# Optimization experiments

Hardware: AMD Instinct MI355X
Metric: run time of the kernel (lower is better)

## Reference

```python
import jax, jax.numpy as jnp
import numpy as np

B, T, F, H = 256, 32, 128, 128
NUM_FILTERS, KH, KW, NUM_CLASSES = 64, 2, 2, 2
FLAT = NUM_FILTERS * (T - KH + 1) * (2 * F - KW + 1)  # 64*31*255 = 505920


def setup_inputs() -> dict:
    key = jax.random.key(0)
    ks = jax.random.split(key, 12)
    inp = {
        "X_nume": jax.random.normal(ks[0], (B, T, F), jnp.float32),
        "att_W": jax.random.uniform(ks[1], (F, H), jnp.float32),
        "att_U": jax.random.uniform(ks[2], (F, H), jnp.float32),
        "att_V": jax.random.uniform(ks[3], (H, 1), jnp.float32),
        "conv_w": jax.random.normal(ks[4], (NUM_FILTERS, 1, KH, KW), jnp.float32) * 0.5,
        "conv_b": jax.random.normal(ks[5], (NUM_FILTERS,), jnp.float32) * 0.1,
        "w1": jax.random.normal(ks[6], (FLAT, 256), jnp.float32) * (1.0 / np.sqrt(FLAT)),
        "b1": jnp.zeros((256,), jnp.float32),
        "w2": jax.random.normal(ks[7], (256, 32), jnp.float32) * (1.0 / np.sqrt(256)),
        "b2": jnp.zeros((32,), jnp.float32),
        "w3": jax.random.normal(ks[8], (32, NUM_CLASSES), jnp.float32) * (1.0 / np.sqrt(32)),
        "b3": jnp.zeros((NUM_CLASSES,), jnp.float32),
    }
    return inp


def reference(X_nume, att_W, att_U, att_V, conv_w, conv_b, w1, b1, w2, b2, w3, b3):
    X = X_nume  # [B, T, F]
    # --- additive attention, fully batched (replaces O(T^2) python loops) ---
    xw = jnp.einsum("btf,fh->bth", X, att_W)  # query proj [B,T,H]
    xu = jnp.einsum("btf,fh->bth", X, att_U)  # key proj   [B,T,H]
    # e[b,i,j] = V^T tanh(x_i W + x_j U)
    scores = jnp.squeeze(jnp.tanh(xw[:, :, None, :] + xu[:, None, :, :]) @ att_V, -1)  # [B,T,T]
    alpha = jax.nn.softmax(scores, axis=-1)  # softmax over j (includes diagonal)
    # context excludes j == i (original skips j == index AFTER softmax)
    mask = 1.0 - jnp.eye(T, dtype=X.dtype)
    c = jnp.einsum("bij,bjf->bif", alpha * mask, X)  # [B,T,F]
    feat = jnp.concatenate([X, c], axis=-1)  # [B,T,2F]
    # --- conv ---
    conv_in = feat[:, None, :, :]  # [B,1,T,2F]
    conv = jax.lax.conv_general_dilated(
        conv_in, conv_w, window_strides=(1, 1), padding="VALID",
        dimension_numbers=("NCHW", "OIHW", "NCHW"))
    conv = jax.nn.relu(conv + conv_b[None, :, None, None])  # [B,64,T-1,2F-1]
    # --- MLP head ---
    flat = conv.reshape(conv.shape[0], -1)
    h = jax.nn.relu(flat @ w1 + b1)
    h = jax.nn.relu(h @ w2 + b2)
    return h @ w3 + b3
```

## Files before the change

kernel.cpp:

```cpp
#include <hip/hip_runtime.h>
#include <hip/hip_bf16.h>

#define B_ 256
#define T_ 32
#define F_ 128
#define H_ 128
#define NF 64
#define OH 31
#define OW 255
#define POS_TOTAL (OH*OW)
#define N1 256
#define KT 248
#define NSTEPS 64

typedef __attribute__((ext_vector_type(8))) short bf16x8;
typedef __attribute__((ext_vector_type(4))) float f32x4;

__device__ __forceinline__ unsigned short f2bf_rne(float f) {
    unsigned int u = __float_as_uint(f);
    u += 0x7FFFu + ((u >> 16) & 1u);
    return (unsigned short)(u >> 16);
}

__global__ __launch_bounds__(256) void k_attn(
    const float* __restrict__ X, const float* __restrict__ W,
    const float* __restrict__ U, const float* __restrict__ V,
    float* __restrict__ featL)
{
    __shared__ float Xs[T_][F_];
    __shared__ float xw[T_][H_];
    __shared__ float xu[T_][H_];
    __shared__ float sc[T_][T_];
    __shared__ float Vs[H_];

    const int b = blockIdx.x;
    const int t = threadIdx.x;
    const float* Xb = X + (size_t)b * T_ * F_;

    for (int idx = t; idx < T_*F_; idx += 256) ((float*)Xs)[idx] = Xb[idx];
    if (t < H_) Vs[t] = V[t];
    __syncthreads();

    {
        const int h = t & 127, half = t >> 7;
        float aw[16], au[16];
        #pragma unroll
        for (int r = 0; r < 16; r++) { aw[r] = 0.f; au[r] = 0.f; }
        for (int f = 0; f < F_; f++) {
            const float wv = W[f*H_ + h];
            const float uv = U[f*H_ + h];
            #pragma unroll
            for (int r = 0; r < 16; r++) {
                const float xv = Xs[half*16 + r][f];
                aw[r] += xv * wv;
                au[r] += xv * uv;
            }
        }
        #pragma unroll
        for (int r = 0; r < 16; r++) {
            xw[half*16 + r][h] = aw[r];
            xu[half*16 + r][h] = au[r];
        }
    }
    __syncthreads();

    {
        const int i = t >> 3;
        const int j0 = (t & 7) * 4;
        float s0 = 0.f, s1 = 0.f, s2 = 0.f, s3 = 0.f;
        for (int h = 0; h < H_; h++) {
            const float xwv = xw[i][h];
            const float vv  = Vs[h];
            s0 += tanhf(xwv + xu[j0+0][h]) * vv;
            s1 += tanhf(xwv + xu[j0+1][h]) * vv;
            s2 += tanhf(xwv + xu[j0+2][h]) * vv;
            s3 += tanhf(xwv + xu[j0+3][h]) * vv;
        }
        sc[i][j0+0] = s0; sc[i][j0+1] = s1; sc[i][j0+2] = s2; sc[i][j0+3] = s3;
    }
    __syncthreads();

    if (t < T_) {
        float m = -1e30f;
        #pragma unroll
        for (int j = 0; j < T_; j++) m = fmaxf(m, sc[t][j]);
        float sum = 0.f;
        #pragma unroll
        for (int j = 0; j < T_; j++) sum += expf(sc[t][j] - m);
        const float inv = 1.f / sum;
        #pragma unroll
        for (int j = 0; j < T_; j++) {
            const float a = expf(sc[t][j] - m) * inv;
            sc[t][j] = (j == t) ? 0.f : a;
        }
    }
    __syncthreads();

    for (int idx = t; idx < T_*F_; idx += 256) {
        const int row = idx >> 7, f = idx & 127;
        float acc = 0.f;
        #pragma unroll
        for (int j = 0; j < T_; j++) acc += sc[row][j] * Xs[j][f];
        float* fr = featL + (size_t)b*8192 + row*256;
        fr[f]       = Xs[row][f];
        fr[128 + f] = acc;
    }
}

__global__ __launch_bounds__(256) void k_tr(
    const float* __restrict__ src, float* __restrict__ dst)
{
    __shared__ float tile[32][33];
    const int rc0 = blockIdx.x * 32;
    const int b0  = blockIdx.y * 32;
    const int tx = threadIdx.x & 31;
    const int ty = threadIdx.x >> 5;
    #pragma unroll
    for (int r = 0; r < 32; r += 8)
        tile[ty + r][tx] = src[(size_t)(b0 + ty + r)*8192 + rc0 + tx];
    __syncthreads();
    #pragma unroll
    for (int r = 0; r < 32; r += 8)
        dst[(size_t)(rc0 + ty + r)*256 + b0 + tx] = tile[tx][ty + r];
}

__global__ __launch_bounds__(512, 2) void k_gemm1(
    const float* __restrict__ featT, const float* __restrict__ cw,
    const float* __restrict__ cb, const float* __restrict__ w1,
    float* __restrict__ partial)
{
    __shared__ unsigned short As[2*4*256*8];
    __shared__ unsigned short Ws[2*4*256*8];
    __shared__ float cwL[256];
    __shared__ float cbL[64];

    const int t  = threadIdx.x;
    const int kt = blockIdx.x;

    if (t < 256) cwL[t] = cw[t];
    if (t < 64)  cbL[t] = cb[t];

    const int rn  = t & 255;
    const int fq2 = t >> 8;

    const int lane = t & 63, wid = t >> 6;
    const int wm = (wid >> 2) * 128;
    const int wn = (wid & 3) * 64;
    const int fr = lane & 15, fq = lane >> 4;

    f32x4 acc[8][4];
    #pragma unroll
    for (int i = 0; i < 8; i++)
        #pragma unroll
        for (int j = 0; j < 4; j++)
            acc[i][j] = (f32x4){0.f, 0.f, 0.f, 0.f};

    float patch[4][8];
    float wvv[2][8];

    const int pb0 = kt * 4;

#define PATCH_LOADS(PB)                                                        \
    {                                                                          \
        const int pbase_ = (PB) * 8;                                           \
        _Pragma("unroll")                                                      \
        for (int pi = 0; pi < 8; pi++) {                                       \
            int pos_ = pbase_ + pi;                                            \
            if (pos_ > POS_TOTAL-1) pos_ = POS_TOTAL-1;                        \
            const int y_ = pos_ / 255;                                         \
            const int x_ = pos_ - y_*255;                                      \
            const float* fp_ = featT + ((size_t)(y_*256 + x_))*256 + rn;       \
            patch[0][pi] = fp_[0];                                             \
            patch[1][pi] = fp_[256];                                           \
            patch[2][pi] = fp_[65536];                                         \
            patch[3][pi] = fp_[65536 + 256];                                   \
        }                                                                      \
    }

#define W_LOADS(SG)                                                            \
    {                                                                          \
        const int fg_ = (SG) & 15;                                             \
        const int pbase_ = (pb0 + ((SG) >> 4)) * 8;                            \
        _Pragma("unroll")                                                      \
        for (int j = 0; j < 2; j++) {                                          \
            const int f_ = fg_*4 + fq2*2 + j;                                  \
            _Pragma("unroll")                                                  \
            for (int pi = 0; pi < 8; pi++) {                                   \
                int pos_ = pbase_ + pi;                                        \
                if (pos_ > POS_TOTAL-1) pos_ = POS_TOTAL-1;                    \
                wvv[j][pi] = w1[(size_t)(f_*POS_TOTAL + pos_)*N1 + rn];        \
            }                                                                  \
        }                                                                      \
    }

#define STAGE_WRITE(BUF, SG)                                                   \
    {                                                                          \
        const int fg_ = (SG) & 15;                                             \
        const int pbase_ = (pb0 + ((SG) >> 4)) * 8;                            \
        _Pragma("unroll")                                                      \
        for (int j = 0; j < 2; j++) {                                          \
            const int f_ = fg_*4 + fq2*2 + j;                                  \
            const float4 cc_ = *(const float4*)&cwL[f_*4];                     \
            const float cbv_ = cbL[f_];                                        \
            unsigned int apk_[4], wpk_[4];                                     \
            _Pragma("unroll")                                                  \
            for (int pi = 0; pi < 8; pi++) {                                   \
                float v_ = patch[0][pi]*cc_.x + patch[1][pi]*cc_.y             \
                         + patch[2][pi]*cc_.z + patch[3][pi]*cc_.w + cbv_;     \
                v_ = (pbase_ + pi < POS_TOTAL) ? fmaxf(v_, 0.f) : 0.f;         \
                const unsigned short ab_ = f2bf_rne(v_);                       \
                const unsigned short wb_ = f2bf_rne(wvv[j][pi]);               \
                if (pi & 1) { apk_[pi>>1] |= (unsigned int)ab_ << 16;          \
                              wpk_[pi>>1] |= (unsigned int)wb_ << 16; }        \
                else        { apk_[pi>>1]  = ab_; wpk_[pi>>1]  = wb_; }        \
            }                                                                  \
            const int blk_ = fq2*2 + j;                                        \
            *(uint4*)&As[(((BUF)*4 + blk_)*256 + rn)*8] = *(uint4*)&apk_[0];   \
            *(uint4*)&Ws[(((BUF)*4 + blk_)*256 + rn)*8] = *(uint4*)&wpk_[0];   \
        }                                                                      \
    }

#define DO_MFMA(BUF)                                                           \
    {                                                                          \
        bf16x8 af_[8], bf_[4];                                                 \
        _Pragma("unroll")                                                      \
        for (int mg = 0; mg < 8; mg++)                                         \
            af_[mg] = *(const bf16x8*)&As[(((BUF)*4 + fq)*256 + wm+mg*16+fr)*8];\
        _Pragma("unroll")                                                      \
        for (int ng = 0; ng < 4; ng++)                                         \
            bf_[ng] = *(const bf16x8*)&Ws[(((BUF)*4 + fq)*256 + wn+ng*16+fr)*8];\
        _Pragma("unroll")                                                      \
        for (int mg = 0; mg < 8; mg++)                                         \
            _Pragma("unroll")                                                  \
            for (int ng = 0; ng < 4; ng++)                                     \
                acc[mg][ng] = __builtin_amdgcn_mfma_f32_16x16x32_bf16(         \
                    af_[mg], bf_[ng], acc[mg][ng], 0, 0, 0);                   \
    }

    PATCH_LOADS(pb0);
    W_LOADS(0);
    __syncthreads();
    STAGE_WRITE(0, 0);
    __syncthreads();

    #pragma unroll 1
    for (int S = 0; S < NSTEPS; S++) {
        const int cur = S & 1;
        if (S + 1 < NSTEPS) {
            if (((S + 1) & 15) == 0) PATCH_LOADS(pb0 + ((S + 1) >> 4));
            W_LOADS(S + 1);
        }
        DO_MFMA(cur);
        if (S + 1 < NSTEPS) STAGE_WRITE(cur ^ 1, S + 1);
        __syncthreads();
    }

    float* pp = partial + (size_t)kt * (256*256);
    #pragma unroll
    for (int mg = 0; mg < 8; mg++)
        #pragma unroll
        for (int ng = 0; ng < 4; ng++) {
            const int col = wn + ng*16 + fr;
            #pragma unroll
            for (int j = 0; j < 4; j++) {
                const int row = wm + mg*16 + fq*4 + j;
                pp[(size_t)row*256 + col] = acc[mg][ng][j];
            }
        }
#undef PATCH_LOADS
#undef W_LOADS
#undef STAGE_WRITE
#undef DO_MFMA
}

__global__ __launch_bounds__(256) void k_head(
    const float* __restrict__ partial, int KT_,
    const float* __restrict__ b1, const float* __restrict__ w2,
    const float* __restrict__ b2, const float* __restrict__ w3,
    const float* __restrict__ b3, float* __restrict__ out)
{
    __shared__ float h1s[256];
    __shared__ float h2s[32];
    const int b = blockIdx.x, t = threadIdx.x;

    float s = b1[t];
    for (int kt = 0; kt < KT_; kt++)
        s += partial[(size_t)kt*(256*N1) + (size_t)b*N1 + t];
    h1s[t] = fmaxf(s, 0.f);
    __syncthreads();

    if (t < 32) {
        float s2 = b2[t];
        for (int i = 0; i < 256; i++) s2 += h1s[i] * w2[i*32 + t];
        h2s[t] = fmaxf(s2, 0.f);
    }
    __syncthreads();

    if (t < 2) {
        float s3 = b3[t];
        #pragma unroll
        for (int i = 0; i < 32; i++) s3 += h2s[i] * w3[i*2 + t];
        out[b*2 + t] = s3;
    }
}

extern "C" void kernel_launch(void* const* d_in, const int* in_sizes, int n_in,
                              void* d_out, int out_size, void* d_ws, size_t ws_size,
                              hipStream_t stream) {
    const float* X    = (const float*)d_in[0];
    const float* attW = (const float*)d_in[1];
    const float* attU = (const float*)d_in[2];
    const float* attV = (const float*)d_in[3];
    const float* cw   = (const float*)d_in[4];
    const float* cb   = (const float*)d_in[5];
    const float* w1   = (const float*)d_in[6];
    const float* b1   = (const float*)d_in[7];
    const float* w2   = (const float*)d_in[8];
    const float* b2   = (const float*)d_in[9];
    const float* w3   = (const float*)d_in[10];
    const float* b3   = (const float*)d_in[11];
    float* out = (float*)d_out;

    float* featL   = (float*)d_ws;
    float* featT   = (float*)((char*)d_ws + (8u<<20));
    float* partial = (float*)((char*)d_ws + (16u<<20));

    k_attn <<<dim3(B_),       dim3(256), 0, stream>>>(X, attW, attU, attV, featL);
    k_tr   <<<dim3(256, 8),   dim3(256), 0, stream>>>(featL, featT);
    k_gemm1<<<dim3(KT),       dim3(512), 0, stream>>>(featT, cw, cb, w1, partial);
    k_head <<<dim3(B_),       dim3(256), 0, stream>>>(partial, KT, b1, w2, b2, w3, b3, out);
}
```

Baseline: 324.3 us.

## Split GEMM1 N dimension across two blocks and deepen weight prefetch pipeline

Each GEMM1 block now covers 128 of the 256 output columns, and the grid doubles to 2×248 blocks. This raises parallelism and cuts per-thread accumulator registers, at the cost of recomputing the conv/ReLU A-tile in both N blocks. The main loop is unrolled by two, with two weight register buffers prefetching further ahead. It uses lighter LDS-only barriers (waitcnt lgkmcnt plus s_barrier) and raises wave priority during the MFMA bursts.

```diff
diff --git a/kernel.cpp b/kernel.cpp
--- a/kernel.cpp
+++ b/kernel.cpp
@@ -22,6 +22,9 @@
     return (unsigned short)(u >> 16);
 }
 
+#define LB() do { asm volatile("s_waitcnt lgkmcnt(0)" ::: "memory"); \
+                  __builtin_amdgcn_s_barrier(); } while (0)
+
 __global__ __launch_bounds__(256) void k_attn(
     const float* __restrict__ X, const float* __restrict__ W,
     const float* __restrict__ U, const float* __restrict__ V,
@@ -129,34 +132,37 @@
     const float* __restrict__ cb, const float* __restrict__ w1,
     float* __restrict__ partial)
 {
-    __shared__ unsigned short As[2*4*256*8];
-    __shared__ unsigned short Ws[2*4*256*8];
+    __shared__ unsigned short As[2][4*256*8];
+    __shared__ unsigned short Ws[2][4*128*8];
     __shared__ float cwL[256];
     __shared__ float cbL[64];
 
     const int t  = threadIdx.x;
-    const int kt = blockIdx.x;
+    const int nt = blockIdx.x;
+    const int kt = blockIdx.y;
+    const int nb = nt * 128;
 
     if (t < 256) cwL[t] = cw[t];
     if (t < 64)  cbL[t] = cb[t];
 
-    const int rn  = t & 255;
-    const int fq2 = t >> 8;
-
+    const int rm = t & 255;
+    const int fh = t >> 8;
+    const int rw = t & 127;
+    const int fw = t >> 7;
     const int lane = t & 63, wid = t >> 6;
-    const int wm = (wid >> 2) * 128;
-    const int wn = (wid & 3) * 64;
+    const int wm = (wid & 3) * 64;
+    const int wn = (wid >> 2) * 64;
     const int fr = lane & 15, fq = lane >> 4;
 
-    f32x4 acc[8][4];
+    f32x4 acc[4][4];
     #pragma unroll
-    for (int i = 0; i < 8; i++)
+    for (int i = 0; i < 4; i++)
         #pragma unroll
         for (int j = 0; j < 4; j++)
             acc[i][j] = (f32x4){0.f, 0.f, 0.f, 0.f};
 
     float patch[4][8];
-    float wvv[2][8];
+    float wvA[8], wvB[8];
 
     const int pb0 = kt * 4;
 
@@ -169,7 +175,7 @@
             if (pos_ > POS_TOTAL-1) pos_ = POS_TOTAL-1;                        \
             const int y_ = pos_ / 255;                                         \
             const int x_ = pos_ - y_*255;                                      \
-            const float* fp_ = featT + ((size_t)(y_*256 + x_))*256 + rn;       \
+            const float* fp_ = featT + ((size_t)(y_*256 + x_))*256 + rm;       \
             patch[0][pi] = fp_[0];                                             \
             patch[1][pi] = fp_[256];                                           \
             patch[2][pi] = fp_[65536];                                         \
@@ -177,99 +183,105 @@
         }                                                                      \
     }
 
-#define W_LOADS(SG)                                                            \
+#define W_LOADS(DST, SG)                                                       \
     {                                                                          \
         const int fg_ = (SG) & 15;                                             \
         const int pbase_ = (pb0 + ((SG) >> 4)) * 8;                            \
-        _Pragma("unroll")                                                      \
-        for (int j = 0; j < 2; j++) {                                          \
-            const int f_ = fg_*4 + fq2*2 + j;                                  \
-            _Pragma("unroll")                                                  \
-            for (int pi = 0; pi < 8; pi++) {                                   \
-                int pos_ = pbase_ + pi;                                        \
-                if (pos_ > POS_TOTAL-1) pos_ = POS_TOTAL-1;                    \
-                wvv[j][pi] = w1[(size_t)(f_*POS_TOTAL + pos_)*N1 + rn];        \
-            }                                                                  \
+        const int f_ = fg_*4 + fw;                                             \
+        _Pragma("unroll")                                                      \
+        for (int pi = 0; pi < 8; pi++) {                                       \
+            int pos_ = pbase_ + pi;                                            \
+            if (pos_ > POS_TOTAL-1) pos_ = POS_TOTAL-1;                        \
+            DST[pi] = w1[(size_t)(f_*POS_TOTAL + pos_)*N1 + nb + rw];          \
         }                                                                      \
     }
 
-#define STAGE_WRITE(BUF, SG)                                                   \
+#define STAGE(BUF, SG, WSRC)                                                   \
     {                                                                          \
         const int fg_ = (SG) & 15;                                             \
         const int pbase_ = (pb0 + ((SG) >> 4)) * 8;                            \
         _Pragma("unroll")                                                      \
         for (int j = 0; j < 2; j++) {                                          \
-            const int f_ = fg_*4 + fq2*2 + j;                                  \
+            const int f_ = fg_*4 + fh*2 + j;                                   \
             const float4 cc_ = *(const float4*)&cwL[f_*4];                     \
             const float cbv_ = cbL[f_];                                        \
-            unsigned int apk_[4], wpk_[4];                                     \
+            unsigned int apk_[4];                                              \
             _Pragma("unroll")                                                  \
             for (int pi = 0; pi < 8; pi++) {                                   \
                 float v_ = patch[0][pi]*cc_.x + patch[1][pi]*cc_.y             \
                          + patch[2][pi]*cc_.z + patch[3][pi]*cc_.w + cbv_;     \
                 v_ = (pbase_ + pi < POS_TOTAL) ? fmaxf(v_, 0.f) : 0.f;         \
                 const unsigned short ab_ = f2bf_rne(v_);                       \
-                const unsigned short wb_ = f2bf_rne(wvv[j][pi]);               \
-                if (pi & 1) { apk_[pi>>1] |= (unsigned int)ab_ << 16;          \
-                              wpk_[pi>>1] |= (unsigned int)wb_ << 16; }        \
-                else        { apk_[pi>>1]  = ab_; wpk_[pi>>1]  = wb_; }        \
+                if (pi & 1) apk_[pi>>1] |= (unsigned int)ab_ << 16;            \
+                else        apk_[pi>>1]  = ab_;                                \
             }                                                                  \
-            const int blk_ = fq2*2 + j;                                        \
-            *(uint4*)&As[(((BUF)*4 + blk_)*256 + rn)*8] = *(uint4*)&apk_[0];   \
-            *(uint4*)&Ws[(((BUF)*4 + blk_)*256 + rn)*8] = *(uint4*)&wpk_[0];   \
+            *(uint4*)&As[BUF][(((fh*2+j)*256) + rm)*8] = *(uint4*)&apk_[0];    \
         }                                                                      \
+        unsigned int wpk_[4];                                                  \
+        _Pragma("unroll")                                                      \
+        for (int pi = 0; pi < 8; pi++) {                                       \
+            const unsigned short wb_ = f2bf_rne(WSRC[pi]);                     \
+            if (pi & 1) wpk_[pi>>1] |= (unsigned int)wb_ << 16;                \
+            else        wpk_[pi>>1]  = wb_;                                    \
+        }                                                                      \
+        *(uint4*)&Ws[BUF][((fw*128) + rw)*8] = *(uint4*)&wpk_[0];              \
     }
 
 #define DO_MFMA(BUF)                                                           \
     {                                                                          \
-        bf16x8 af_[8], bf_[4];                                                 \
-        _Pragma("unroll")                                                      \
-        for (int mg = 0; mg < 8; mg++)                                         \
-            af_[mg] = *(const bf16x8*)&As[(((BUF)*4 + fq)*256 + wm+mg*16+fr)*8];\
+        bf16x8 af_[4], bf_[4];                                                 \
+        _Pragma("unroll")                                                      \
+        for (int mg = 0; mg < 4; mg++)                                         \
+            af_[mg] = *(const bf16x8*)&As[BUF][((fq*256) + wm+mg*16+fr)*8];    \
         _Pragma("unroll")                                                      \
         for (int ng = 0; ng < 4; ng++)                                         \
-            bf_[ng] = *(const bf16x8*)&Ws[(((BUF)*4 + fq)*256 + wn+ng*16+fr)*8];\
-        _Pragma("unroll")                                                      \
-        for (int mg = 0; mg < 8; mg++)                                         \
+            bf_[ng] = *(const bf16x8*)&Ws[BUF][((fq*128) + wn+ng*16+fr)*8];    \
+        __builtin_amdgcn_s_setprio(1);                                         \
+        _Pragma("unroll")                                                      \
+        for (int mg = 0; mg < 4; mg++)                                         \
             _Pragma("unroll")                                                  \
             for (int ng = 0; ng < 4; ng++)                                     \
                 acc[mg][ng] = __builtin_amdgcn_mfma_f32_16x16x32_bf16(         \
                     af_[mg], bf_[ng], acc[mg][ng], 0, 0, 0);                   \
+        __builtin_amdgcn_s_setprio(0);                                         \
     }
 
     PATCH_LOADS(pb0);
-    W_LOADS(0);
-    __syncthreads();
-    STAGE_WRITE(0, 0);
-    __syncthreads();
+    W_LOADS(wvA, 0);
+    W_LOADS(wvB, 1);
+    __syncthreads();
+    STAGE(0, 0, wvA);
+    LB();
 
     #pragma unroll 1
-    for (int S = 0; S < NSTEPS; S++) {
-        const int cur = S & 1;
-        if (S + 1 < NSTEPS) {
-            if (((S + 1) & 15) == 0) PATCH_LOADS(pb0 + ((S + 1) >> 4));
-            W_LOADS(S + 1);
-        }
-        DO_MFMA(cur);
-        if (S + 1 < NSTEPS) STAGE_WRITE(cur ^ 1, S + 1);
-        __syncthreads();
-    }
-
-    float* pp = partial + (size_t)kt * (256*256);
+    for (int g = 0; g < 32; g++) {
+        const int S = 2*g;
+        if (g < 31) W_LOADS(wvA, S+2);
+        DO_MFMA(0);
+        STAGE(1, S+1, wvB);
+        if (g < 31 && ((S+2) & 15) == 0) PATCH_LOADS(pb0 + ((S+2) >> 4));
+        if (g < 31) W_LOADS(wvB, S+3);
+        LB();
+        DO_MFMA(1);
+        if (g < 31) STAGE(0, S+2, wvA);
+        LB();
+    }
+
+    float* pp = partial + (size_t)kt * (256*N1) + nb;
     #pragma unroll
-    for (int mg = 0; mg < 8; mg++)
+    for (int mg = 0; mg < 4; mg++)
         #pragma unroll
         for (int ng = 0; ng < 4; ng++) {
             const int col = wn + ng*16 + fr;
             #pragma unroll
             for (int j = 0; j < 4; j++) {
                 const int row = wm + mg*16 + fq*4 + j;
-                pp[(size_t)row*256 + col] = acc[mg][ng][j];
+                pp[(size_t)row*N1 + col] = acc[mg][ng][j];
             }
         }
 #undef PATCH_LOADS
 #undef W_LOADS
-#undef STAGE_WRITE
+#undef STAGE
 #undef DO_MFMA
 }
 
@@ -327,6 +339,6 @@
 
     k_attn <<<dim3(B_),       dim3(256), 0, stream>>>(X, attW, attU, attV, featL);
     k_tr   <<<dim3(256, 8),   dim3(256), 0, stream>>>(featL, featT);
-    k_gemm1<<<dim3(KT),       dim3(512), 0, stream>>>(featT, cw, cb, w1, partial);
+    k_gemm1<<<dim3(2, KT),    dim3(512), 0, stream>>>(featT, cw, cb, w1, partial);
     k_head <<<dim3(B_),       dim3(256), 0, stream>>>(partial, KT, b1, w2, b2, w3, b3, out);
 }
```

Result: slower. 403.7 us (+24.5%).
